# Performance work log

Measured on AMD Instinct MI355X. Metric: run time of the kernel, lower is better.

## Reference

```python
import jax, jax.numpy as jnp
import numpy as np

CLASSES = 128
M_IN = 64
N_OUT = 32
N_SAMPLES = 65536


def setup_inputs() -> dict:
    key = jax.random.key(0)
    k1, k2, k3, k4 = jax.random.split(key, 4)
    x = jax.random.normal(k1, (N_SAMPLES, M_IN), dtype=jnp.float32)
    inds = jax.random.randint(k2, (N_SAMPLES,), 0, CLASSES, dtype=jnp.int64)
    # Conv2d(in=M_IN, out=CLASSES*N_OUT, kernel=1) -> weight (CLASSES*N_OUT, M_IN), bias (CLASSES*N_OUT,)
    bound = 1.0 / np.sqrt(M_IN)
    W = jax.random.uniform(k3, (CLASSES * N_OUT, M_IN), minval=-bound, maxval=bound, dtype=jnp.float32)
    b = jax.random.uniform(k4, (CLASSES * N_OUT,), minval=-bound, maxval=bound, dtype=jnp.float32)
    return {"x": x, "inds": inds, "W": W, "b": b}


def reference(x, inds, W, b):
    # 1x1 conv == GEMM: (N, m) @ (m, classes*n) + bias -> (N, classes*n)
    y = jnp.einsum("nm,cm->nc", x, W) + b  # (N, classes*n_out)
    y = y.reshape(-1, CLASSES, N_OUT)       # (N, classes, n_out)
    # gather the selected class slice per sample
    idx = inds.astype(jnp.int32)[:, None, None]  # (N, 1, 1)
    out = jnp.take_along_axis(y, jnp.broadcast_to(idx, (y.shape[0], 1, N_OUT)), axis=1)
    return out.reshape(-1, N_OUT)
```

## Files before the change

### kernel.cpp

```cpp
#include <hip/hip_runtime.h>

#define CLASSES    128
#define M_IN       64
#define N_OUT      32
#define N_SAMPLES  65536

#define G      64
#define CAP_G  40
#define CAP_L  768

typedef __attribute__((ext_vector_type(8))) short bf16x8;
typedef __attribute__((ext_vector_type(4))) float f32x4;

__device__ inline short f2bf(float f) {
    unsigned u = __builtin_bit_cast(unsigned, f);
    u += 0x7fffu + ((u >> 16) & 1u);
    return (short)(u >> 16);
}

__device__ inline bf16x8 cvt8(const float4 a, const float4 b) {
    bf16x8 r;
    r[0] = f2bf(a.x); r[1] = f2bf(a.y); r[2] = f2bf(a.z); r[3] = f2bf(a.w);
    r[4] = f2bf(b.x); r[5] = f2bf(b.y); r[6] = f2bf(b.z); r[7] = f2bf(b.w);
    return r;
}

__global__ __launch_bounds__(256) void scatter_kernel(
    const int* __restrict__ inds,
    int*       __restrict__ counts,
    int*       __restrict__ bucket)
{
    __shared__ int lcnt[CLASSES];
    const int tid = threadIdx.x;
    const int g   = blockIdx.x;
    if (tid < CLASSES) lcnt[tid] = 0;
    __syncthreads();

    const int4 v  = reinterpret_cast<const int4*>(inds)[g * 256 + tid];
    const int  i0 = (g * 256 + tid) * 4;
    const int  p0 = atomicAdd(&lcnt[v.x], 1);
    const int  p1 = atomicAdd(&lcnt[v.y], 1);
    const int  p2 = atomicAdd(&lcnt[v.z], 1);
    const int  p3 = atomicAdd(&lcnt[v.w], 1);
    __syncthreads();

    if (tid < CLASSES) counts[tid * G + g] = lcnt[tid];

    if (p0 < CAP_G) bucket[(v.x * G + g) * CAP_G + p0] = i0;
    if (p1 < CAP_G) bucket[(v.y * G + g) * CAP_G + p1] = i0 + 1;
    if (p2 < CAP_G) bucket[(v.z * G + g) * CAP_G + p2] = i0 + 2;
    if (p3 < CAP_G) bucket[(v.w * G + g) * CAP_G + p3] = i0 + 3;
}

__global__ __launch_bounds__(256) void compute_kernel(
    const float* __restrict__ x,
    const float* __restrict__ W,
    const float* __restrict__ b,
    const int*   __restrict__ counts,
    const int*   __restrict__ bucket,
    float*       __restrict__ out)
{
    const int tid  = threadIdx.x;
    const int c    = blockIdx.x >> 2;
    const int j4   = blockIdx.x & 3;
    const int wv   = tid >> 6;
    const int lane = tid & 63;
    const int m16  = lane & 15;
    const int quad = lane >> 4;

    __shared__ int flist[CAP_L];
    __shared__ int shTot;

    bf16x8 Bf[2][2];
#pragma unroll
    for (int nh = 0; nh < 2; ++nh)
#pragma unroll
        for (int kh = 0; kh < 2; ++kh) {
            const float* p = W + (size_t)(c * N_OUT + nh * 16 + m16) * M_IN
                               + kh * 32 + quad * 8;
            Bf[nh][kh] = cvt8(*(const float4*)p, *(const float4*)(p + 4));
        }
    const float b0 = b[c * N_OUT + m16];
    const float b1 = b[c * N_OUT + 16 + m16];

    if (wv == 0) {
        const int cntg = counts[c * G + lane];
        int s = cntg;
#pragma unroll
        for (int off = 1; off < 64; off <<= 1) {
            const int o = __shfl_up(s, off, 64);
            if (lane >= off) s += o;
        }
        const int excl = s - cntg;
        const int* seg = bucket + (c * G + lane) * CAP_G;
        for (int i = 0; i < cntg; ++i) {
            const int d = excl + i;
            if (d < CAP_L) flist[d] = seg[i];
        }
        if (lane == 63) shTot = (s < CAP_L) ? s : CAP_L;
    }
    __syncthreads();

    const int cn = shTot;
    if (cn == 0) return;
    const int T = (cn + 15) >> 4;
    int t = j4 * 4 + wv;
    if (t >= T) return;

    int base = t << 4;
    int pa = base + m16;
    int na = flist[(pa < cn) ? pa : (cn - 1)];
    const float* xr = x + (size_t)na * M_IN + quad * 8;
    float4 xa0 = *(const float4*)xr,        xa1 = *(const float4*)(xr + 4);
    float4 xa2 = *(const float4*)(xr + 32), xa3 = *(const float4*)(xr + 36);

    while (true) {
        const int  tn   = t + 16;
        const bool more = tn < T;

        int base_n = base, na_n = na;
        float4 xb0 = xa0, xb1 = xa1, xb2 = xa2, xb3 = xa3;
        if (more) {
            base_n = tn << 4;
            const int pan = base_n + m16;
            na_n = flist[(pan < cn) ? pan : (cn - 1)];
            const float* xrn = x + (size_t)na_n * M_IN + quad * 8;
            xb0 = *(const float4*)xrn;        xb1 = *(const float4*)(xrn + 4);
            xb2 = *(const float4*)(xrn + 32); xb3 = *(const float4*)(xrn + 36);
        }

        const bf16x8 A0 = cvt8(xa0, xa1);
        const bf16x8 A1 = cvt8(xa2, xa3);
        f32x4 acc0 = {0.f, 0.f, 0.f, 0.f};
        f32x4 acc1 = {0.f, 0.f, 0.f, 0.f};
        acc0 = __builtin_amdgcn_mfma_f32_16x16x32_bf16(A0, Bf[0][0], acc0, 0, 0, 0);
        acc0 = __builtin_amdgcn_mfma_f32_16x16x32_bf16(A1, Bf[0][1], acc0, 0, 0, 0);
        acc1 = __builtin_amdgcn_mfma_f32_16x16x32_bf16(A0, Bf[1][0], acc1, 0, 0, 0);
        acc1 = __builtin_amdgcn_mfma_f32_16x16x32_bf16(A1, Bf[1][1], acc1, 0, 0, 0);

#pragma unroll
        for (int r = 0; r < 4; ++r) {
            const int p = base + quad * 4 + r;
            if (p < cn) {
                const int n = flist[p];
                out[(size_t)n * N_OUT + m16]      = acc0[r] + b0;
                out[(size_t)n * N_OUT + 16 + m16] = acc1[r] + b1;
            }
        }

        if (!more) break;
        t = tn; base = base_n; na = na_n;
        xa0 = xb0; xa1 = xb1; xa2 = xb2; xa3 = xb3;
    }
}

extern "C" void kernel_launch(void* const* d_in, const int* in_sizes, int n_in,
                              void* d_out, int out_size, void* d_ws, size_t ws_size,
                              hipStream_t stream) {
    const float* x    = (const float*)d_in[0];
    const int*   inds = (const int*)  d_in[1];
    const float* W    = (const float*)d_in[2];
    const float* bia  = (const float*)d_in[3];
    float*       out  = (float*)d_out;

    int* counts = (int*)d_ws;
    int* bucket = (int*)d_ws + CLASSES * G;

    scatter_kernel<<<G,           256, 0, stream>>>(inds, counts, bucket);
    compute_kernel<<<CLASSES * 4, 256, 0, stream>>>(x, W, bia, counts, bucket, out);
}
```

Baseline: 79.09 us.

## Fuse scatter and compute kernels with a global flag barrier

Merges the index-bucketing kernel into the compute kernel. The first 64 blocks do the scatter and then publish per-group release flags, and every block spin-waits on those flags before building its class list. This removes one kernel launch and the gap between the two kernels. It also spreads the flist gather across all four waves instead of one. The cost is a grid-wide spin dependency that relies on the first 64 blocks being co-resident. The flags use a magic value that is not reset between calls, so a stale value left in the workspace from a previous run could let blocks pass before the current scatter has finished.

```diff
diff --git a/kernel.cpp b/kernel.cpp
--- a/kernel.cpp
+++ b/kernel.cpp
@@ -25,39 +25,14 @@
     return r;
 }
 
-__global__ __launch_bounds__(256) void scatter_kernel(
-    const int* __restrict__ inds,
-    int*       __restrict__ counts,
-    int*       __restrict__ bucket)
-{
-    __shared__ int lcnt[CLASSES];
-    const int tid = threadIdx.x;
-    const int g   = blockIdx.x;
-    if (tid < CLASSES) lcnt[tid] = 0;
-    __syncthreads();
-
-    const int4 v  = reinterpret_cast<const int4*>(inds)[g * 256 + tid];
-    const int  i0 = (g * 256 + tid) * 4;
-    const int  p0 = atomicAdd(&lcnt[v.x], 1);
-    const int  p1 = atomicAdd(&lcnt[v.y], 1);
-    const int  p2 = atomicAdd(&lcnt[v.z], 1);
-    const int  p3 = atomicAdd(&lcnt[v.w], 1);
-    __syncthreads();
-
-    if (tid < CLASSES) counts[tid * G + g] = lcnt[tid];
-
-    if (p0 < CAP_G) bucket[(v.x * G + g) * CAP_G + p0] = i0;
-    if (p1 < CAP_G) bucket[(v.y * G + g) * CAP_G + p1] = i0 + 1;
-    if (p2 < CAP_G) bucket[(v.z * G + g) * CAP_G + p2] = i0 + 2;
-    if (p3 < CAP_G) bucket[(v.w * G + g) * CAP_G + p3] = i0 + 3;
-}
-
-__global__ __launch_bounds__(256) void compute_kernel(
+__global__ __launch_bounds__(256) void fused_kernel(
     const float* __restrict__ x,
+    const int*   __restrict__ inds,
     const float* __restrict__ W,
     const float* __restrict__ b,
-    const int*   __restrict__ counts,
-    const int*   __restrict__ bucket,
+    int*         __restrict__ counts,
+    int*         __restrict__ bucket,
+    int*         __restrict__ flags,
     float*       __restrict__ out)
 {
     const int tid  = threadIdx.x;
@@ -68,8 +43,8 @@
     const int m16  = lane & 15;
     const int quad = lane >> 4;
 
+    __shared__ int lcnt[CLASSES];
     __shared__ int flist[CAP_L];
-    __shared__ int shTot;
 
     bf16x8 Bf[2][2];
 #pragma unroll
@@ -83,25 +58,64 @@
     const float b0 = b[c * N_OUT + m16];
     const float b1 = b[c * N_OUT + 16 + m16];
 
+    if (blockIdx.x < G) {
+        const int g = blockIdx.x;
+        if (tid < CLASSES) lcnt[tid] = 0;
+        __syncthreads();
+
+        const int4 v  = reinterpret_cast<const int4*>(inds)[g * 256 + tid];
+        const int  i0 = (g * 256 + tid) * 4;
+        const int  p0 = atomicAdd(&lcnt[v.x], 1);
+        const int  p1 = atomicAdd(&lcnt[v.y], 1);
+        const int  p2 = atomicAdd(&lcnt[v.z], 1);
+        const int  p3 = atomicAdd(&lcnt[v.w], 1);
+        __syncthreads();
+
+        if (tid < CLASSES) counts[tid * G + g] = lcnt[tid];
+        if (p0 < CAP_G) bucket[(v.x * G + g) * CAP_G + p0] = i0;
+        if (p1 < CAP_G) bucket[(v.y * G + g) * CAP_G + p1] = i0 + 1;
+        if (p2 < CAP_G) bucket[(v.z * G + g) * CAP_G + p2] = i0 + 2;
+        if (p3 < CAP_G) bucket[(v.w * G + g) * CAP_G + p3] = i0 + 3;
+
+        __threadfence();
+        __syncthreads();
+        if (tid == 0)
+            __hip_atomic_store(&flags[g * 16], 0x5A170000 | g,
+                               __ATOMIC_RELEASE, __HIP_MEMORY_SCOPE_AGENT);
+    }
+
     if (wv == 0) {
-        const int cntg = counts[c * G + lane];
-        int s = cntg;
-#pragma unroll
-        for (int off = 1; off < 64; off <<= 1) {
-            const int o = __shfl_up(s, off, 64);
-            if (lane >= off) s += o;
+        const int target = 0x5A170000 | lane;
+        while (__hip_atomic_load(&flags[lane * 16],
+                                 __ATOMIC_ACQUIRE, __HIP_MEMORY_SCOPE_AGENT)
+               != target) {
+            __builtin_amdgcn_s_sleep(7);
         }
-        const int excl = s - cntg;
-        const int* seg = bucket + (c * G + lane) * CAP_G;
-        for (int i = 0; i < cntg; ++i) {
-            const int d = excl + i;
-            if (d < CAP_L) flist[d] = seg[i];
-        }
-        if (lane == 63) shTot = (s < CAP_L) ? s : CAP_L;
     }
     __syncthreads();
 
-    const int cn = shTot;
+    const int cg = counts[c * G + lane];
+    int s = cg;
+#pragma unroll
+    for (int off = 1; off < 64; off <<= 1) {
+        const int o = __shfl_up(s, off, 64);
+        if (lane >= off) s += o;
+    }
+    const int excl  = s - cg;
+    const int total = __shfl(s, 63, 64);
+
+    const int sgid   = wv * 16 + (lane >> 2);
+    const int sub    = lane & 3;
+    const int cnt_s  = __shfl(cg,   sgid & 63, 64);
+    const int excl_s = __shfl(excl, sgid & 63, 64);
+    const int* seg = bucket + (size_t)(c * G + sgid) * CAP_G;
+    for (int i = sub; i < cnt_s; i += 4) {
+        const int d = excl_s + i;
+        if (d < CAP_L) flist[d] = seg[i];
+    }
+    __syncthreads();
+
+    const int cn = (total < CAP_L) ? total : CAP_L;
     if (cn == 0) return;
     const int T = (cn + 15) >> 4;
     int t = j4 * 4 + wv;
@@ -164,8 +178,9 @@
     float*       out  = (float*)d_out;
 
     int* counts = (int*)d_ws;
-    int* bucket = (int*)d_ws + CLASSES * G;
+    int* bucket = counts + CLASSES * G;
+    int* flags  = bucket + CLASSES * G * CAP_G;
 
-    scatter_kernel<<<G,           256, 0, stream>>>(inds, counts, bucket);
-    compute_kernel<<<CLASSES * 4, 256, 0, stream>>>(x, W, bia, counts, bucket, out);
+    fused_kernel<<<CLASSES * 4, 256, 0, stream>>>(x, inds, W, bia,
+                                                  counts, bucket, flags, out);
 }
```

Result: slower. 125.4 us (+58.5%).
